# Kernel optimization log

Hardware: AMD Instinct MI355X
Metric: run time of the kernel (lower is better)

The kernel has to match this reference:

```python
import jax, jax.numpy as jnp
import numpy as np

B, S, DIM = 1, 2048, 4096
NH, NKV, HD = 32, 8, 128  # n_head, n_local_heads (kv heads), head_dim
ROPE_BASE = 10000.0


def setup_inputs() -> dict:
    key = jax.random.key(0)
    k1, k2, k3 = jax.random.split(key, 3)
    x = jax.random.normal(k1, (B, S, DIM), dtype=jnp.float32)
    total_head_dim = (NH + 2 * NKV) * HD  # 6144
    wqkv = jax.random.normal(k2, (total_head_dim, DIM), dtype=jnp.float32) * 0.02
    wo = jax.random.normal(k3, (DIM, DIM), dtype=jnp.float32) * 0.02
    # standard RoPE table: (S, HD//2, 2) = (cos, sin)
    inv_freq = 1.0 / (ROPE_BASE ** (np.arange(0, HD, 2, dtype=np.float32) / HD))
    ang = np.outer(np.arange(S, dtype=np.float32), inv_freq)
    freqs_cis = jnp.asarray(np.stack([np.cos(ang), np.sin(ang)], axis=-1), dtype=jnp.float32)
    return {"x": x, "freqs_cis": freqs_cis, "wqkv": wqkv, "wo": wo}


def _apply_rotary(x, freqs_cis):
    # x: (b, s, h, d); freqs_cis: (s, d//2, 2)
    b, s, h, d = x.shape
    xs = x.reshape(b, s, h, d // 2, 2)
    fc = freqs_cis.reshape(1, s, 1, d // 2, 2)
    re = xs[..., 0] * fc[..., 0] - xs[..., 1] * fc[..., 1]
    im = xs[..., 0] * fc[..., 1] + xs[..., 1] * fc[..., 0]
    return jnp.stack([re, im], axis=-1).reshape(b, s, h, d)


def reference(x, freqs_cis, wqkv, wo):
    b, s, _ = x.shape
    kv_size = NKV * HD
    qkv = x @ wqkv.T  # (b, s, (NH+2*NKV)*HD)
    q, k, v = jnp.split(qkv, [NH * HD, NH * HD + kv_size], axis=-1)
    q = q.reshape(b, s, NH, HD)
    k = k.reshape(b, s, NKV, HD)
    v = v.reshape(b, s, NKV, HD)
    q = _apply_rotary(q, freqs_cis)
    k = _apply_rotary(k, freqs_cis)
    rep = NH // NKV  # GQA expansion factor; repeat_kv == grouped einsum below
    qg = q.reshape(b, s, NKV, rep, HD)
    scale = 1.0 / jnp.sqrt(jnp.asarray(HD, q.dtype))
    # scores: (b, g, r, q_pos, k_pos) -- avoids materializing repeated K/V
    scores = jnp.einsum('bqgrd,bkgd->bgrqk', qg, k) * scale
    causal = jnp.tril(jnp.ones((s, s), dtype=bool))
    scores = jnp.where(causal, scores, jnp.finfo(scores.dtype).min)
    p = jax.nn.softmax(scores, axis=-1)
    o = jnp.einsum('bgrqk,bkgd->bqgrd', p, v).reshape(b, s, NH * HD)
    return o @ wo.T
```

## Files before the change

### kernel.cpp

```cpp
#include <hip/hip_runtime.h>
#include <hip/hip_bf16.h>
#include <math.h>


typedef __attribute__((ext_vector_type(8))) __bf16 bf16x8;
typedef __attribute__((ext_vector_type(4))) float f32x4;

#define NEG_BIG (-1e30f)

#define ASYNC_CP16(gsrc, ldst)                                                            \
  __builtin_amdgcn_global_load_lds((const __attribute__((address_space(1))) void*)(gsrc), \
                                   (__attribute__((address_space(3))) void*)(ldst), 16, 0, 0)

__device__ __forceinline__ f32x4 mfma_bf16(bf16x8 a, bf16x8 b, f32x4 c) {
  return __builtin_amdgcn_mfma_f32_16x16x32_bf16(a, b, c, 0, 0, 0);
}

__device__ __forceinline__ float clampf(float v) {
  return fminf(fmaxf(v, -30000.f), 30000.f);
}

__device__ __forceinline__ bf16x8 ldg8(const __hip_bfloat16* p) {
  return *(const bf16x8*)p;
}
__device__ __forceinline__ bf16x8 ldg8(const float* p) {
  f32x4 a = *(const f32x4*)p;
  f32x4 b = *(const f32x4*)(p + 4);
  bf16x8 r;
  r[0] = (__bf16)a[0]; r[1] = (__bf16)a[1]; r[2] = (__bf16)a[2]; r[3] = (__bf16)a[3];
  r[4] = (__bf16)b[0]; r[5] = (__bf16)b[1]; r[6] = (__bf16)b[2]; r[7] = (__bf16)b[3];
  return r;
}

__device__ __forceinline__ void store_c(float* C, size_t idx, float v) {
  C[idx] = clampf(v);
}
__device__ __forceinline__ void store_c(__hip_bfloat16* C, size_t idx, float v) {
  C[idx] = __float2bfloat16(clampf(v));
}

__global__ __launch_bounds__(256) void cvt_f32_bf16(const float* __restrict__ src,
                                                    __hip_bfloat16* __restrict__ dst) {
  size_t i = ((size_t)blockIdx.x * 256 + threadIdx.x) * 8;
  *(bf16x8*)&dst[i] = ldg8(src + i);
}

template <typename TA, typename TB, typename TC>
__global__ __launch_bounds__(256) void gemm_nt(
    const TA* __restrict__ A, const TB* __restrict__ B,
    TC* __restrict__ C, int M, int N, int K) {
  __shared__ __align__(16) __hip_bfloat16 As[128 * 32];
  __shared__ __align__(16) __hip_bfloat16 Bs[128 * 32];
  const int tid = threadIdx.x;
  const int lane = tid & 63, wave = tid >> 6;
  const int l15 = lane & 15, quad = lane >> 4;
  const int wm = (wave >> 1) * 64, wn = (wave & 1) * 64;
  const size_t mBase = (size_t)blockIdx.y * 128, nBase = (size_t)blockIdx.x * 128;

  const int ldRow = tid >> 2;
  const int ldCol = (tid & 3) * 8;
  const TA* Ap = A + (mBase + ldRow) * (size_t)K + ldCol;
  const TB* Bp = B + (nBase + ldRow) * (size_t)K + ldCol;

  f32x4 acc[4][4] = {};

  for (int k0 = 0; k0 < K; k0 += 32) {
    bf16x8 a0 = ldg8(Ap);
    bf16x8 a1 = ldg8(Ap + (size_t)64 * K);
    bf16x8 b0 = ldg8(Bp);
    bf16x8 b1 = ldg8(Bp + (size_t)64 * K);
    Ap += 32; Bp += 32;
    *(bf16x8*)&As[tid * 8] = a0;
    *(bf16x8*)&As[2048 + tid * 8] = a1;
    *(bf16x8*)&Bs[tid * 8] = b0;
    *(bf16x8*)&Bs[2048 + tid * 8] = b1;
    __syncthreads();
    bf16x8 af[4], bfr[4];
#pragma unroll
    for (int i = 0; i < 4; i++)
      af[i] = *(const bf16x8*)&As[(wm + i * 16 + l15) * 32 + quad * 8];
#pragma unroll
    for (int j = 0; j < 4; j++)
      bfr[j] = *(const bf16x8*)&Bs[(wn + j * 16 + l15) * 32 + quad * 8];
#pragma unroll
    for (int i = 0; i < 4; i++)
#pragma unroll
      for (int j = 0; j < 4; j++)
        acc[i][j] = mfma_bf16(af[i], bfr[j], acc[i][j]);
    __syncthreads();
  }

#pragma unroll
  for (int i = 0; i < 4; i++)
#pragma unroll
    for (int j = 0; j < 4; j++)
#pragma unroll
      for (int r = 0; r < 4; r++) {
        size_t row = mBase + wm + i * 16 + quad * 4 + r;
        size_t col = nBase + wn + j * 16 + l15;
        store_c(C, row * (size_t)N + col, acc[i][j][r]);
      }
}

template <typename TC>
__global__ __launch_bounds__(256) void gemm_nt_async(
    const __hip_bfloat16* __restrict__ A, const __hip_bfloat16* __restrict__ B,
    TC* __restrict__ C, int M, int N, int K) {
  __shared__ __align__(16) __hip_bfloat16 As[128 * 32];
  __shared__ __align__(16) __hip_bfloat16 Bs[128 * 32];
  const int tid = threadIdx.x;
  const int lane = tid & 63, wave = tid >> 6;
  const int l15 = lane & 15, quad = lane >> 4;
  const int wm = (wave >> 1) * 64, wn = (wave & 1) * 64;
  const size_t mBase = (size_t)blockIdx.y * 128, nBase = (size_t)blockIdx.x * 128;

  const int ldRow = tid >> 2;
  const int ldCol = (tid & 3) * 8;
  const __hip_bfloat16* Ap = A + (mBase + ldRow) * (size_t)K + ldCol;
  const __hip_bfloat16* Bp = B + (nBase + ldRow) * (size_t)K + ldCol;

  f32x4 acc[4][4] = {};

  for (int k0 = 0; k0 < K; k0 += 32) {
    ASYNC_CP16(Ap, &As[tid * 8]);
    ASYNC_CP16(Ap + (size_t)64 * K, &As[2048 + tid * 8]);
    ASYNC_CP16(Bp, &Bs[tid * 8]);
    ASYNC_CP16(Bp + (size_t)64 * K, &Bs[2048 + tid * 8]);
    Ap += 32; Bp += 32;
    __syncthreads();
    bf16x8 af[4], bfr[4];
#pragma unroll
    for (int i = 0; i < 4; i++)
      af[i] = *(const bf16x8*)&As[(wm + i * 16 + l15) * 32 + quad * 8];
#pragma unroll
    for (int j = 0; j < 4; j++)
      bfr[j] = *(const bf16x8*)&Bs[(wn + j * 16 + l15) * 32 + quad * 8];
#pragma unroll
    for (int i = 0; i < 4; i++)
#pragma unroll
      for (int j = 0; j < 4; j++)
        acc[i][j] = mfma_bf16(af[i], bfr[j], acc[i][j]);
    __syncthreads();
  }

#pragma unroll
  for (int i = 0; i < 4; i++)
#pragma unroll
    for (int j = 0; j < 4; j++)
#pragma unroll
      for (int r = 0; r < 4; r++) {
        size_t row = mBase + wm + i * 16 + quad * 4 + r;
        size_t col = nBase + wn + j * 16 + l15;
        store_c(C, row * (size_t)N + col, acc[i][j][r]);
      }
}

__global__ __launch_bounds__(256) void rope_kernel(__hip_bfloat16* __restrict__ qkv,
                                                   const float* __restrict__ fc) {
  int idx = blockIdx.x * 256 + threadIdx.x;
  int d = idx & 63;
  int h = (idx >> 6) % 40;
  int s = idx / (40 * 64);
  size_t off = (size_t)s * 6144 + h * 128 + d * 2;
  float x0 = __bfloat162float(qkv[off]);
  float x1 = __bfloat162float(qkv[off + 1]);
  float c = fc[s * 128 + d * 2];
  float sn = fc[s * 128 + d * 2 + 1];
  qkv[off] = __float2bfloat16(x0 * c - x1 * sn);
  qkv[off + 1] = __float2bfloat16(x0 * sn + x1 * c);
}

__global__ __launch_bounds__(256) void transpose_v(const __hip_bfloat16* __restrict__ qkv,
                                                   __hip_bfloat16* __restrict__ vt) {
  __shared__ __hip_bfloat16 tile[32][33];
  int x = threadIdx.x & 31, y = threadIdx.x >> 5;
  int colBase = blockIdx.x * 32;
  int sBase = blockIdx.y * 32;
#pragma unroll
  for (int i = 0; i < 4; i++)
    tile[y + i * 8][x] = qkv[(size_t)(sBase + y + i * 8) * 6144 + 5120 + colBase + x];
  __syncthreads();
#pragma unroll
  for (int i = 0; i < 4; i++)
    vt[(size_t)(colBase + y + i * 8) * 2048 + sBase + x] = tile[x][y + i * 8];
}

__global__ __launch_bounds__(256) void flash_attn(
    const __hip_bfloat16* __restrict__ qkv, const __hip_bfloat16* __restrict__ vt,
    __hip_bfloat16* __restrict__ o) {
  __shared__ __align__(16) __hip_bfloat16 Ks[64 * 128];
  __shared__ __align__(16) __hip_bfloat16 Vs[128 * 64];
  __shared__ __align__(16) __hip_bfloat16 Ps[4][16 * 72];
  const int tid = threadIdx.x;
  const int lane = tid & 63, wave = tid >> 6;
  const int l15 = lane & 15, quad = lane >> 4;
  const int h = blockIdx.y, g = h >> 2;
  const int qBase = blockIdx.x * 64;
  const int qRow = qBase + wave * 16;

  bf16x8 qf[4];
  {
    const __hip_bfloat16* qp = qkv + (size_t)(qRow + l15) * 6144 + h * 128 + quad * 8;
#pragma unroll
    for (int d = 0; d < 4; d++) qf[d] = *(const bf16x8*)(qp + d * 32);
  }

  f32x4 acc_o[8] = {};
  float m_i[4], l_i[4];
#pragma unroll
  for (int r = 0; r < 4; r++) { m_i[r] = NEG_BIG; l_i[r] = 0.f; }

  const float scale = 0.08838834764831845f;
  const int nkt = blockIdx.x + 1;
  for (int kt = 0; kt < nkt; kt++) {
    const int kBase = kt * 64;
#pragma unroll
    for (int rnd = 0; rnd < 4; rnd++) {
      int ci = rnd * 256 + tid;
      int row = ci >> 4, chl = ci & 15;
      int chg = chl ^ (row & 15);
      ASYNC_CP16(qkv + (size_t)(kBase + row) * 6144 + 4096 + g * 128 + chg * 8, &Ks[ci * 8]);
    }
#pragma unroll
    for (int rnd = 0; rnd < 4; rnd++) {
      int ci = rnd * 256 + tid;
      int n = ci >> 3, chl = ci & 7;
      int chg = chl ^ (n & 7);
      ASYNC_CP16(vt + (size_t)(g * 128 + n) * 2048 + kBase + chg * 8, &Vs[ci * 8]);
    }
    __syncthreads();

    f32x4 sc[4] = {};
#pragma unroll
    for (int d = 0; d < 4; d++) {
#pragma unroll
      for (int j = 0; j < 4; j++) {
        bf16x8 kb = *(const bf16x8*)&Ks[(j * 16 + l15) * 128 + ((d * 4 + quad) ^ l15) * 8];
        sc[j] = mfma_bf16(qf[d], kb, sc[j]);
      }
    }

    float rowmax[4] = {NEG_BIG, NEG_BIG, NEG_BIG, NEG_BIG};
    float sv[4][4];
#pragma unroll
    for (int j = 0; j < 4; j++) {
      int kcol = kBase + j * 16 + l15;
#pragma unroll
      for (int r = 0; r < 4; r++) {
        float s = clampf(sc[j][r] * scale);
        if (kcol > qRow + quad * 4 + r) s = NEG_BIG;
        sv[j][r] = s;
        rowmax[r] = fmaxf(rowmax[r], s);
      }
    }
#pragma unroll
    for (int off = 8; off; off >>= 1)
#pragma unroll
      for (int r = 0; r < 4; r++)
        rowmax[r] = fmaxf(rowmax[r], __shfl_xor(rowmax[r], off, 16));

    float alpha[4], rowsum[4];
#pragma unroll
    for (int r = 0; r < 4; r++) {
      float mnew = fmaxf(m_i[r], rowmax[r]);
      alpha[r] = __expf(m_i[r] - mnew);
      m_i[r] = mnew;
      rowsum[r] = 0.f;
    }
#pragma unroll
    for (int j = 0; j < 4; j++)
#pragma unroll
      for (int r = 0; r < 4; r++) {
        float p = __expf(sv[j][r] - m_i[r]);
        rowsum[r] += p;
        Ps[wave][(quad * 4 + r) * 72 + j * 16 + l15] = __float2bfloat16(p);
      }
#pragma unroll
    for (int off = 8; off; off >>= 1)
#pragma unroll
      for (int r = 0; r < 4; r++)
        rowsum[r] += __shfl_xor(rowsum[r], off, 16);
#pragma unroll
    for (int r = 0; r < 4; r++) l_i[r] = l_i[r] * alpha[r] + rowsum[r];

#pragma unroll
    for (int jt = 0; jt < 8; jt++)
#pragma unroll
      for (int r = 0; r < 4; r++) acc_o[jt][r] *= alpha[r];

    __syncthreads();

#pragma unroll
    for (int kk = 0; kk < 2; kk++) {
      bf16x8 pa = *(const bf16x8*)&Ps[wave][l15 * 72 + kk * 32 + quad * 8];
#pragma unroll
      for (int jt = 0; jt < 8; jt++) {
        int n = jt * 16 + l15;
        bf16x8 vb = *(const bf16x8*)&Vs[n * 64 + (((kk * 4 + quad) ^ (n & 7))) * 8];
        acc_o[jt] = mfma_bf16(pa, vb, acc_o[jt]);
      }
    }
    __syncthreads();
  }

#pragma unroll
  for (int r = 0; r < 4; r++) {
    float inv = 1.f / l_i[r];
    size_t qr = qRow + quad * 4 + r;
#pragma unroll
    for (int jt = 0; jt < 8; jt++)
      o[qr * 4096 + h * 128 + jt * 16 + l15] = __float2bfloat16(clampf(acc_o[jt][r] * inv));
  }
}

extern "C" void kernel_launch(void* const* d_in, const int* in_sizes, int n_in,
                              void* d_out, int out_size, void* d_ws, size_t ws_size,
                              hipStream_t stream) {
  const float* x = (const float*)d_in[0];
  const float* fc = (const float*)d_in[1];
  const float* wqkv = (const float*)d_in[2];
  const float* wo = (const float*)d_in[3];
  float* out = (float*)d_out;

  char* ws = (char*)d_ws;
  __hip_bfloat16* qkv = (__hip_bfloat16*)ws;
  __hip_bfloat16* vt  = (__hip_bfloat16*)(ws + 25165824);
  __hip_bfloat16* ob  = (__hip_bfloat16*)(ws + 29360128);
  __hip_bfloat16* xb  = (__hip_bfloat16*)(ws + 46137344);
  __hip_bfloat16* wb  = (__hip_bfloat16*)(ws + 62914560);

  const bool fast = ws_size >= (size_t)113246208;

  if (fast) {
    cvt_f32_bf16<<<dim3(4096), 256, 0, stream>>>(x, xb);
    cvt_f32_bf16<<<dim3(12288), 256, 0, stream>>>(wqkv, wb);
    gemm_nt_async<__hip_bfloat16>
        <<<dim3(48, 16), 256, 0, stream>>>(xb, wb, qkv, 2048, 6144, 4096);
  } else {
    gemm_nt<float, float, __hip_bfloat16>
        <<<dim3(48, 16), 256, 0, stream>>>(x, wqkv, qkv, 2048, 6144, 4096);
  }
  rope_kernel<<<dim3(20480), 256, 0, stream>>>(qkv, fc);
  transpose_v<<<dim3(32, 64), 256, 0, stream>>>(qkv, vt);
  flash_attn<<<dim3(32, 32), 256, 0, stream>>>(qkv, vt, ob);
  if (fast) {
    cvt_f32_bf16<<<dim3(8192), 256, 0, stream>>>(wo, wb);
    gemm_nt_async<float>
        <<<dim3(32, 16), 256, 0, stream>>>(ob, wb, out, 2048, 4096, 4096);
  } else {
    gemm_nt<__hip_bfloat16, float, float>
        <<<dim3(32, 16), 256, 0, stream>>>(ob, wo, out, 2048, 4096, 4096);
  }
}
```

Measured before the change: 634.0 us.

## Fuse RoPE and V-transpose into QKV GEMM epilogue; widen attention tiles

The QKV GEMM epilogue now applies rotary embedding to Q/K columns and writes V columns directly in transposed layout. This removes the separate rope and transpose kernels along with their extra global memory passes. Flash attention now processes 128 query rows per block, with two 16-row tiles per wave sharing each K/V load, and schedules the heaviest causal blocks first. The wider tiles raise register pressure, halve the grid size, and interleave both softmax tiles through a single per-wave P buffer.

```diff
diff --git a/kernel.cpp b/kernel.cpp
--- a/kernel.cpp
+++ b/kernel.cpp
@@ -4,6 +4,7 @@
 
 
 typedef __attribute__((ext_vector_type(8))) __bf16 bf16x8;
+typedef __attribute__((ext_vector_type(4))) __bf16 bf16x4;
 typedef __attribute__((ext_vector_type(4))) float f32x4;
 
 #define NEG_BIG (-1e30f)
@@ -43,6 +44,128 @@
                                                     __hip_bfloat16* __restrict__ dst) {
   size_t i = ((size_t)blockIdx.x * 256 + threadIdx.x) * 8;
   *(bf16x8*)&dst[i] = ldg8(src + i);
+}
+
+__global__ __launch_bounds__(256) void gemm_qkv_rope(
+    const __hip_bfloat16* __restrict__ A, const __hip_bfloat16* __restrict__ B,
+    __hip_bfloat16* __restrict__ qkv, __hip_bfloat16* __restrict__ vt,
+    const float* __restrict__ fc) {
+  const int K = 4096;
+  __shared__ __align__(16) __hip_bfloat16 As[128 * 32];
+  __shared__ __align__(16) __hip_bfloat16 Bs[128 * 32];
+  const int tid = threadIdx.x;
+  const int lane = tid & 63, wave = tid >> 6;
+  const int l15 = lane & 15, quad = lane >> 4;
+  const int wm = (wave >> 1) * 64, wn = (wave & 1) * 64;
+  const size_t mBase = (size_t)blockIdx.y * 128, nBase = (size_t)blockIdx.x * 128;
+
+  const int ldRow = tid >> 2;
+  const int ldCol = (tid & 3) * 8;
+  const __hip_bfloat16* Ap = A + (mBase + ldRow) * (size_t)K + ldCol;
+  const __hip_bfloat16* Bp = B + (nBase + ldRow) * (size_t)K + ldCol;
+
+  f32x4 acc[4][4] = {};
+
+  for (int k0 = 0; k0 < K; k0 += 32) {
+    ASYNC_CP16(Ap, &As[tid * 8]);
+    ASYNC_CP16(Ap + (size_t)64 * K, &As[2048 + tid * 8]);
+    ASYNC_CP16(Bp, &Bs[tid * 8]);
+    ASYNC_CP16(Bp + (size_t)64 * K, &Bs[2048 + tid * 8]);
+    Ap += 32; Bp += 32;
+    __syncthreads();
+    bf16x8 af[4], bfr[4];
+#pragma unroll
+    for (int i = 0; i < 4; i++)
+      af[i] = *(const bf16x8*)&As[(wm + i * 16 + l15) * 32 + quad * 8];
+#pragma unroll
+    for (int j = 0; j < 4; j++)
+      bfr[j] = *(const bf16x8*)&Bs[(wn + j * 16 + l15) * 32 + quad * 8];
+#pragma unroll
+    for (int i = 0; i < 4; i++)
+#pragma unroll
+      for (int j = 0; j < 4; j++)
+        acc[i][j] = mfma_bf16(af[i], bfr[j], acc[i][j]);
+    __syncthreads();
+  }
+
+#pragma unroll
+  for (int i = 0; i < 4; i++)
+#pragma unroll
+    for (int j = 0; j < 4; j++) {
+      size_t c = nBase + wn + j * 16 + l15;
+      size_t srow0 = mBase + wm + i * 16 + quad * 4;
+      if (c < 5120) {
+        int di2 = (int)(c & 126);
+#pragma unroll
+        for (int r = 0; r < 4; r++) {
+          float v = clampf(acc[i][j][r]);
+          float vp = __shfl_xor(v, 1);
+          size_t s = srow0 + r;
+          float cs = fc[s * 128 + di2];
+          float sn = fc[s * 128 + di2 + 1];
+          float ov = ((c & 1) == 0) ? (v * cs - vp * sn) : (vp * sn + v * cs);
+          qkv[s * 6144 + c] = __float2bfloat16(ov);
+        }
+      } else {
+        bf16x4 pk;
+#pragma unroll
+        for (int r = 0; r < 4; r++) pk[r] = (__bf16)clampf(acc[i][j][r]);
+        *(bf16x4*)&vt[(c - 5120) * 2048 + srow0] = pk;
+      }
+    }
+}
+
+template <typename TC>
+__global__ __launch_bounds__(256) void gemm_nt_async(
+    const __hip_bfloat16* __restrict__ A, const __hip_bfloat16* __restrict__ B,
+    TC* __restrict__ C, int M, int N, int K) {
+  __shared__ __align__(16) __hip_bfloat16 As[128 * 32];
+  __shared__ __align__(16) __hip_bfloat16 Bs[128 * 32];
+  const int tid = threadIdx.x;
+  const int lane = tid & 63, wave = tid >> 6;
+  const int l15 = lane & 15, quad = lane >> 4;
+  const int wm = (wave >> 1) * 64, wn = (wave & 1) * 64;
+  const size_t mBase = (size_t)blockIdx.y * 128, nBase = (size_t)blockIdx.x * 128;
+
+  const int ldRow = tid >> 2;
+  const int ldCol = (tid & 3) * 8;
+  const __hip_bfloat16* Ap = A + (mBase + ldRow) * (size_t)K + ldCol;
+  const __hip_bfloat16* Bp = B + (nBase + ldRow) * (size_t)K + ldCol;
+
+  f32x4 acc[4][4] = {};
+
+  for (int k0 = 0; k0 < K; k0 += 32) {
+    ASYNC_CP16(Ap, &As[tid * 8]);
+    ASYNC_CP16(Ap + (size_t)64 * K, &As[2048 + tid * 8]);
+    ASYNC_CP16(Bp, &Bs[tid * 8]);
+    ASYNC_CP16(Bp + (size_t)64 * K, &Bs[2048 + tid * 8]);
+    Ap += 32; Bp += 32;
+    __syncthreads();
+    bf16x8 af[4], bfr[4];
+#pragma unroll
+    for (int i = 0; i < 4; i++)
+      af[i] = *(const bf16x8*)&As[(wm + i * 16 + l15) * 32 + quad * 8];
+#pragma unroll
+    for (int j = 0; j < 4; j++)
+      bfr[j] = *(const bf16x8*)&Bs[(wn + j * 16 + l15) * 32 + quad * 8];
+#pragma unroll
+    for (int i = 0; i < 4; i++)
+#pragma unroll
+      for (int j = 0; j < 4; j++)
+        acc[i][j] = mfma_bf16(af[i], bfr[j], acc[i][j]);
+    __syncthreads();
+  }
+
+#pragma unroll
+  for (int i = 0; i < 4; i++)
+#pragma unroll
+    for (int j = 0; j < 4; j++)
+#pragma unroll
+      for (int r = 0; r < 4; r++) {
+        size_t row = mBase + wm + i * 16 + quad * 4 + r;
+        size_t col = nBase + wn + j * 16 + l15;
+        store_c(C, row * (size_t)N + col, acc[i][j][r]);
+      }
 }
 
 template <typename TA, typename TB, typename TC>
@@ -56,14 +179,11 @@
   const int l15 = lane & 15, quad = lane >> 4;
   const int wm = (wave >> 1) * 64, wn = (wave & 1) * 64;
   const size_t mBase = (size_t)blockIdx.y * 128, nBase = (size_t)blockIdx.x * 128;
-
   const int ldRow = tid >> 2;
   const int ldCol = (tid & 3) * 8;
   const TA* Ap = A + (mBase + ldRow) * (size_t)K + ldCol;
   const TB* Bp = B + (nBase + ldRow) * (size_t)K + ldCol;
-
   f32x4 acc[4][4] = {};
-
   for (int k0 = 0; k0 < K; k0 += 32) {
     bf16x8 a0 = ldg8(Ap);
     bf16x8 a1 = ldg8(Ap + (size_t)64 * K);
@@ -89,60 +209,6 @@
         acc[i][j] = mfma_bf16(af[i], bfr[j], acc[i][j]);
     __syncthreads();
   }
-
-#pragma unroll
-  for (int i = 0; i < 4; i++)
-#pragma unroll
-    for (int j = 0; j < 4; j++)
-#pragma unroll
-      for (int r = 0; r < 4; r++) {
-        size_t row = mBase + wm + i * 16 + quad * 4 + r;
-        size_t col = nBase + wn + j * 16 + l15;
-        store_c(C, row * (size_t)N + col, acc[i][j][r]);
-      }
-}
-
-template <typename TC>
-__global__ __launch_bounds__(256) void gemm_nt_async(
-    const __hip_bfloat16* __restrict__ A, const __hip_bfloat16* __restrict__ B,
-    TC* __restrict__ C, int M, int N, int K) {
-  __shared__ __align__(16) __hip_bfloat16 As[128 * 32];
-  __shared__ __align__(16) __hip_bfloat16 Bs[128 * 32];
-  const int tid = threadIdx.x;
-  const int lane = tid & 63, wave = tid >> 6;
-  const int l15 = lane & 15, quad = lane >> 4;
-  const int wm = (wave >> 1) * 64, wn = (wave & 1) * 64;
-  const size_t mBase = (size_t)blockIdx.y * 128, nBase = (size_t)blockIdx.x * 128;
-
-  const int ldRow = tid >> 2;
-  const int ldCol = (tid & 3) * 8;
-  const __hip_bfloat16* Ap = A + (mBase + ldRow) * (size_t)K + ldCol;
-  const __hip_bfloat16* Bp = B + (nBase + ldRow) * (size_t)K + ldCol;
-
-  f32x4 acc[4][4] = {};
-
-  for (int k0 = 0; k0 < K; k0 += 32) {
-    ASYNC_CP16(Ap, &As[tid * 8]);
-    ASYNC_CP16(Ap + (size_t)64 * K, &As[2048 + tid * 8]);
-    ASYNC_CP16(Bp, &Bs[tid * 8]);
-    ASYNC_CP16(Bp + (size_t)64 * K, &Bs[2048 + tid * 8]);
-    Ap += 32; Bp += 32;
-    __syncthreads();
-    bf16x8 af[4], bfr[4];
-#pragma unroll
-    for (int i = 0; i < 4; i++)
-      af[i] = *(const bf16x8*)&As[(wm + i * 16 + l15) * 32 + quad * 8];
-#pragma unroll
-    for (int j = 0; j < 4; j++)
-      bfr[j] = *(const bf16x8*)&Bs[(wn + j * 16 + l15) * 32 + quad * 8];
-#pragma unroll
-    for (int i = 0; i < 4; i++)
-#pragma unroll
-      for (int j = 0; j < 4; j++)
-        acc[i][j] = mfma_bf16(af[i], bfr[j], acc[i][j]);
-    __syncthreads();
-  }
-
 #pragma unroll
   for (int i = 0; i < 4; i++)
 #pragma unroll
@@ -194,24 +260,29 @@
   const int tid = threadIdx.x;
   const int lane = tid & 63, wave = tid >> 6;
   const int l15 = lane & 15, quad = lane >> 4;
-  const int h = blockIdx.y, g = h >> 2;
-  const int qBase = blockIdx.x * 64;
-  const int qRow = qBase + wave * 16;
-
-  bf16x8 qf[4];
-  {
-    const __hip_bfloat16* qp = qkv + (size_t)(qRow + l15) * 6144 + h * 128 + quad * 8;
-#pragma unroll
-    for (int d = 0; d < 4; d++) qf[d] = *(const bf16x8*)(qp + d * 32);
-  }
-
-  f32x4 acc_o[8] = {};
-  float m_i[4], l_i[4];
-#pragma unroll
-  for (int r = 0; r < 4; r++) { m_i[r] = NEG_BIG; l_i[r] = 0.f; }
+  const int h = blockIdx.x, g = h >> 2;
+  const int qt = 15 - blockIdx.y;
+  const int qBase = qt * 128;
+  const int qRowW = qBase + wave * 32;
+
+  bf16x8 qf[2][4];
+#pragma unroll
+  for (int t = 0; t < 2; t++) {
+    const __hip_bfloat16* qp =
+        qkv + (size_t)(qRowW + t * 16 + l15) * 6144 + h * 128 + quad * 8;
+#pragma unroll
+    for (int d = 0; d < 4; d++) qf[t][d] = *(const bf16x8*)(qp + d * 32);
+  }
+
+  f32x4 acc_o[2][8] = {};
+  float m_i[2][4], l_i[2][4];
+#pragma unroll
+  for (int t = 0; t < 2; t++)
+#pragma unroll
+    for (int r = 0; r < 4; r++) { m_i[t][r] = NEG_BIG; l_i[t][r] = 0.f; }
 
   const float scale = 0.08838834764831845f;
-  const int nkt = blockIdx.x + 1;
+  const int nkt = 2 * qt + 2;
   for (int kt = 0; kt < nkt; kt++) {
     const int kBase = kt * 64;
 #pragma unroll
@@ -230,87 +301,93 @@
     }
     __syncthreads();
 
-    f32x4 sc[4] = {};
+    f32x4 sc[2][4] = {};
 #pragma unroll
     for (int d = 0; d < 4; d++) {
 #pragma unroll
       for (int j = 0; j < 4; j++) {
         bf16x8 kb = *(const bf16x8*)&Ks[(j * 16 + l15) * 128 + ((d * 4 + quad) ^ l15) * 8];
-        sc[j] = mfma_bf16(qf[d], kb, sc[j]);
-      }
-    }
-
-    float rowmax[4] = {NEG_BIG, NEG_BIG, NEG_BIG, NEG_BIG};
-    float sv[4][4];
-#pragma unroll
-    for (int j = 0; j < 4; j++) {
-      int kcol = kBase + j * 16 + l15;
+        sc[0][j] = mfma_bf16(qf[0][d], kb, sc[0][j]);
+        sc[1][j] = mfma_bf16(qf[1][d], kb, sc[1][j]);
+      }
+    }
+
+#pragma unroll
+    for (int t = 0; t < 2; t++) {
+      const int qRowT = qRowW + t * 16;
+      float rowmax[4] = {NEG_BIG, NEG_BIG, NEG_BIG, NEG_BIG};
+      float sv[4][4];
+#pragma unroll
+      for (int j = 0; j < 4; j++) {
+        int kcol = kBase + j * 16 + l15;
+#pragma unroll
+        for (int r = 0; r < 4; r++) {
+          float s = clampf(sc[t][j][r] * scale);
+          if (kcol > qRowT + quad * 4 + r) s = NEG_BIG;
+          sv[j][r] = s;
+          rowmax[r] = fmaxf(rowmax[r], s);
+        }
+      }
+#pragma unroll
+      for (int off = 8; off; off >>= 1)
+#pragma unroll
+        for (int r = 0; r < 4; r++)
+          rowmax[r] = fmaxf(rowmax[r], __shfl_xor(rowmax[r], off, 16));
+
+      float alpha[4], rowsum[4];
 #pragma unroll
       for (int r = 0; r < 4; r++) {
-        float s = clampf(sc[j][r] * scale);
-        if (kcol > qRow + quad * 4 + r) s = NEG_BIG;
-        sv[j][r] = s;
-        rowmax[r] = fmaxf(rowmax[r], s);
-      }
-    }
-#pragma unroll
-    for (int off = 8; off; off >>= 1)
-#pragma unroll
-      for (int r = 0; r < 4; r++)
-        rowmax[r] = fmaxf(rowmax[r], __shfl_xor(rowmax[r], off, 16));
-
-    float alpha[4], rowsum[4];
+        float mnew = fmaxf(m_i[t][r], rowmax[r]);
+        alpha[r] = __expf(m_i[t][r] - mnew);
+        m_i[t][r] = mnew;
+        rowsum[r] = 0.f;
+      }
+#pragma unroll
+      for (int j = 0; j < 4; j++)
+#pragma unroll
+        for (int r = 0; r < 4; r++) {
+          float p = __expf(sv[j][r] - m_i[t][r]);
+          rowsum[r] += p;
+          Ps[wave][(quad * 4 + r) * 72 + j * 16 + l15] = __float2bfloat16(p);
+        }
+#pragma unroll
+      for (int off = 8; off; off >>= 1)
+#pragma unroll
+        for (int r = 0; r < 4; r++)
+          rowsum[r] += __shfl_xor(rowsum[r], off, 16);
+#pragma unroll
+      for (int r = 0; r < 4; r++) l_i[t][r] = l_i[t][r] * alpha[r] + rowsum[r];
+
+#pragma unroll
+      for (int jt = 0; jt < 8; jt++)
+#pragma unroll
+        for (int r = 0; r < 4; r++) acc_o[t][jt][r] *= alpha[r];
+
+#pragma unroll
+      for (int kk = 0; kk < 2; kk++) {
+        bf16x8 pa = *(const bf16x8*)&Ps[wave][l15 * 72 + kk * 32 + quad * 8];
+#pragma unroll
+        for (int jt = 0; jt < 8; jt++) {
+          int n = jt * 16 + l15;
+          bf16x8 vb = *(const bf16x8*)&Vs[n * 64 + (((kk * 4 + quad) ^ (n & 7))) * 8];
+          acc_o[t][jt] = mfma_bf16(pa, vb, acc_o[t][jt]);
+        }
+      }
+    }
+    __syncthreads();
+  }
+
+#pragma unroll
+  for (int t = 0; t < 2; t++)
 #pragma unroll
     for (int r = 0; r < 4; r++) {
-      float mnew = fmaxf(m_i[r], rowmax[r]);
-      alpha[r] = __expf(m_i[r] - mnew);
-      m_i[r] = mnew;
-      rowsum[r] = 0.f;
-    }
-#pragma unroll
-    for (int j = 0; j < 4; j++)
-#pragma unroll
-      for (int r = 0; r < 4; r++) {
-        float p = __expf(sv[j][r] - m_i[r]);
-        rowsum[r] += p;
-        Ps[wave][(quad * 4 + r) * 72 + j * 16 + l15] = __float2bfloat16(p);
-      }
-#pragma unroll
-    for (int off = 8; off; off >>= 1)
-#pragma unroll
-      for (int r = 0; r < 4; r++)
-        rowsum[r] += __shfl_xor(rowsum[r], off, 16);
-#pragma unroll
-    for (int r = 0; r < 4; r++) l_i[r] = l_i[r] * alpha[r] + rowsum[r];
-
-#pragma unroll
-    for (int jt = 0; jt < 8; jt++)
-#pragma unroll
-      for (int r = 0; r < 4; r++) acc_o[jt][r] *= alpha[r];
-
-    __syncthreads();
-
-#pragma unroll
-    for (int kk = 0; kk < 2; kk++) {
-      bf16x8 pa = *(const bf16x8*)&Ps[wave][l15 * 72 + kk * 32 + quad * 8];
-#pragma unroll
-      for (int jt = 0; jt < 8; jt++) {
-        int n = jt * 16 + l15;
-        bf16x8 vb = *(const bf16x8*)&Vs[n * 64 + (((kk * 4 + quad) ^ (n & 7))) * 8];
-        acc_o[jt] = mfma_bf16(pa, vb, acc_o[jt]);
-      }
-    }
-    __syncthreads();
-  }
-
-#pragma unroll
-  for (int r = 0; r < 4; r++) {
-    float inv = 1.f / l_i[r];
-    size_t qr = qRow + quad * 4 + r;
-#pragma unroll
-    for (int jt = 0; jt < 8; jt++)
-      o[qr * 4096 + h * 128 + jt * 16 + l15] = __float2bfloat16(clampf(acc_o[jt][r] * inv));
-  }
+      float inv = 1.f / l_i[t][r];
+      size_t qr = qRowW + t * 16 + quad * 4 + r;
+#pragma unroll
+      for (int jt = 0; jt < 8; jt++)
+        o[qr * 4096 + h * 128 + jt * 16 + l15] =
+            __float2bfloat16(clampf(acc_o[t][jt][r] * inv));
+    }
 }
 
 extern "C" void kernel_launch(void* const* d_in, const int* in_sizes, int n_in,
@@ -334,15 +411,14 @@
   if (fast) {
     cvt_f32_bf16<<<dim3(4096), 256, 0, stream>>>(x, xb);
     cvt_f32_bf16<<<dim3(12288), 256, 0, stream>>>(wqkv, wb);
-    gemm_nt_async<__hip_bfloat16>
-        <<<dim3(48, 16), 256, 0, stream>>>(xb, wb, qkv, 2048, 6144, 4096);
+    gemm_qkv_rope<<<dim3(48, 16), 256, 0, stream>>>(xb, wb, qkv, vt, fc);
   } else {
     gemm_nt<float, float, __hip_bfloat16>
         <<<dim3(48, 16), 256, 0, stream>>>(x, wqkv, qkv, 2048, 6144, 4096);
-  }
-  rope_kernel<<<dim3(20480), 256, 0, stream>>>(qkv, fc);
-  transpose_v<<<dim3(32, 64), 256, 0, stream>>>(qkv, vt);
-  flash_attn<<<dim3(32, 32), 256, 0, stream>>>(qkv, vt, ob);
+    rope_kernel<<<dim3(20480), 256, 0, stream>>>(qkv, fc);
+    transpose_v<<<dim3(32, 64), 256, 0, stream>>>(qkv, vt);
+  }
+  flash_attn<<<dim3(32, 16), 256, 0, stream>>>(qkv, vt, ob);
   if (fast) {
     cvt_f32_bf16<<<dim3(8192), 256, 0, stream>>>(wo, wb);
     gemm_nt_async<float>
```

Result: faster. 553.2 us (-12.7%).
